# Optimization experiments

Measured on AMD Instinct MI355X. Metric: run time of the kernel, lower is better.

Reference implementation:

```python
import jax, jax.numpy as jnp
import numpy as np

M = 50000   # eval points
N = 1024    # gaussians
EPS = 1e-6


def setup_inputs() -> dict:
    key = jax.random.key(0)
    k1, k2, k3 = jax.random.split(key, 3)
    points = jax.random.uniform(k1, (M, 3), dtype=jnp.float32)          # normalized coords in [0,1)
    positions = jax.random.uniform(k2, (N, 3), dtype=jnp.float32)       # torch.rand init
    log_scales = jnp.full((N, 3), -3.0, dtype=jnp.float32)              # torch.full(..., -3.0)
    intensities = jax.random.uniform(k3, (N,), dtype=jnp.float32) * 0.5  # torch.rand * 0.5
    return {"points": points, "positions": positions,
            "log_scales": log_scales, "intensities": intensities}


def reference(points, positions, log_scales, intensities):
    # Faithful translation of FastGaussianModel._eval_gaussians
    scales = jnp.exp(log_scales)                      # [N,3]
    inv_var = 1.0 / (scales ** 2 + EPS)               # [N,3]
    diff = points[:, None, :] - positions[None, :, :] # [M,N,3]
    quad = jnp.einsum('mnd,nd->mn', diff * diff, inv_var)  # [M,N]
    gauss = jnp.exp(-0.5 * quad)                      # [M,N]
    values = gauss @ intensities                      # [M]
    return values
```

## Files before the change

kernel.cpp:

```cpp
#include <hip/hip_runtime.h>


typedef float v2f __attribute__((ext_vector_type(2)));

constexpr int NG_CHUNK = 128;
constexpr int BLOCK    = 256;

__global__ void fgm_prep(const float* __restrict__ positions,
                         const float* __restrict__ log_scales,
                         const float* __restrict__ intensities,
                         float* __restrict__ coef, int N, int Npad) {
    int n = blockIdx.x * blockDim.x + threadIdx.x;
    if (n >= Npad) return;
    float a0=0.f, a1=0.f, a2=0.f, b0=0.f, b1=0.f, b2=0.f, c=0.f, w=0.f;
    if (n < N) {
        const float K = -0.7213475204444817f;
        float q0 = positions[3*n+0], q1 = positions[3*n+1], q2 = positions[3*n+2];
        float iv0 = 1.0f / (__expf(2.0f*log_scales[3*n+0]) + 1e-6f);
        float iv1 = 1.0f / (__expf(2.0f*log_scales[3*n+1]) + 1e-6f);
        float iv2 = 1.0f / (__expf(2.0f*log_scales[3*n+2]) + 1e-6f);
        a0 = K * (-2.f*iv0*q0);  b0 = K * iv0;
        a1 = K * (-2.f*iv1*q1);  b1 = K * iv1;
        a2 = K * (-2.f*iv2*q2);  b2 = K * iv2;
        c  = K * (iv0*q0*q0 + iv1*q1*q1 + iv2*q2*q2);
        w  = intensities[n];
    }
    coef[0*Npad+n] = a0;  coef[1*Npad+n] = a1;  coef[2*Npad+n] = a2;
    coef[3*Npad+n] = b0;  coef[4*Npad+n] = b1;  coef[5*Npad+n] = b2;
    coef[6*Npad+n] = c;   coef[7*Npad+n] = w;
}

__global__ __launch_bounds__(BLOCK) void fgm_main(const float* __restrict__ points,
                                                  const float* __restrict__ coef,
                                                  float* __restrict__ out,
                                                  int M, int Npad) {
    int m = blockIdx.x * blockDim.x + threadIdx.x;
    float px = 0.f, py = 0.f, pz = 0.f;
    if (m < M) {
        px = points[3*m+0];
        py = points[3*m+1];
        pz = points[3*m+2];
    }
    v2f vpx  = {px, px},       vpy  = {py, py},       vpz  = {pz, pz};
    v2f vpx2 = {px*px, px*px}, vpy2 = {py*py, py*py}, vpz2 = {pz*pz, pz*pz};

    int half = blockIdx.y * (NG_CHUNK/2);
    const v2f* A0 = (const v2f*)(coef + 0*Npad) + half;
    const v2f* A1 = (const v2f*)(coef + 1*Npad) + half;
    const v2f* A2 = (const v2f*)(coef + 2*Npad) + half;
    const v2f* B0 = (const v2f*)(coef + 3*Npad) + half;
    const v2f* B1 = (const v2f*)(coef + 4*Npad) + half;
    const v2f* B2 = (const v2f*)(coef + 5*Npad) + half;
    const v2f* C  = (const v2f*)(coef + 6*Npad) + half;
    const v2f* W  = (const v2f*)(coef + 7*Npad) + half;

    v2f acc = {0.f, 0.f};
    #pragma unroll 4
    for (int i = 0; i < NG_CHUNK/2; ++i) {
        v2f t = __builtin_elementwise_fma(A0[i], vpx,  C[i]);
        t = __builtin_elementwise_fma(A1[i], vpy,  t);
        t = __builtin_elementwise_fma(A2[i], vpz,  t);
        t = __builtin_elementwise_fma(B0[i], vpx2, t);
        t = __builtin_elementwise_fma(B1[i], vpy2, t);
        t = __builtin_elementwise_fma(B2[i], vpz2, t);
        v2f g;
        g.x = __builtin_amdgcn_exp2f(t.x);
        g.y = __builtin_amdgcn_exp2f(t.y);
        acc = __builtin_elementwise_fma(g, W[i], acc);
    }
    if (m < M) atomicAdd(&out[m], acc.x + acc.y);
}

extern "C" void kernel_launch(void* const* d_in, const int* in_sizes, int n_in,
                              void* d_out, int out_size, void* d_ws, size_t ws_size,
                              hipStream_t stream) {
    const float* points      = (const float*)d_in[0];
    const float* positions   = (const float*)d_in[1];
    const float* log_scales  = (const float*)d_in[2];
    const float* intensities = (const float*)d_in[3];
    int M = in_sizes[0] / 3;
    int N = in_sizes[3];

    int chunks = (N + NG_CHUNK - 1) / NG_CHUNK;
    int Npad   = chunks * NG_CHUNK;

    float* coef = (float*)d_ws;

    hipMemsetAsync(d_out, 0, (size_t)out_size * sizeof(float), stream);

    fgm_prep<<<(Npad + 255) / 256, 256, 0, stream>>>(positions, log_scales,
                                                     intensities, coef, N, Npad);

    dim3 grid((M + BLOCK - 1) / BLOCK, chunks);
    fgm_main<<<grid, BLOCK, 0, stream>>>(points, coef, (float*)d_out, M, Npad);
}
```

Baseline: 77.07 us.

## Interleave coefficients per gaussian pair and drop N-splitting with atomics

The prep kernel now packs the eight coefficients of each gaussian pair contiguously as four float4s, so the main loop reads one contiguous 64-byte record per iteration instead of eight separate streams. The main kernel no longer splits the gaussians across a second grid dimension. Each 64-thread block loops over all pairs and writes its result directly, which removes the memset and the atomicAdds. The cost is a much smaller grid (about 782 single-wave blocks for 256 CUs) and longer per-thread loops, which reduces latency hiding and parallelism.

After: 105.2 us. +36.4%, slower.

```diff
diff --git a/kernel.cpp b/kernel.cpp
--- a/kernel.cpp
+++ b/kernel.cpp
@@ -3,38 +3,45 @@
 
 typedef float v2f __attribute__((ext_vector_type(2)));
 
-constexpr int NG_CHUNK = 128;
-constexpr int BLOCK    = 256;
+constexpr int BLOCK = 64;
 
 __global__ void fgm_prep(const float* __restrict__ positions,
                          const float* __restrict__ log_scales,
                          const float* __restrict__ intensities,
-                         float* __restrict__ coef, int N, int Npad) {
-    int n = blockIdx.x * blockDim.x + threadIdx.x;
-    if (n >= Npad) return;
-    float a0=0.f, a1=0.f, a2=0.f, b0=0.f, b1=0.f, b2=0.f, c=0.f, w=0.f;
-    if (n < N) {
-        const float K = -0.7213475204444817f;
-        float q0 = positions[3*n+0], q1 = positions[3*n+1], q2 = positions[3*n+2];
-        float iv0 = 1.0f / (__expf(2.0f*log_scales[3*n+0]) + 1e-6f);
-        float iv1 = 1.0f / (__expf(2.0f*log_scales[3*n+1]) + 1e-6f);
-        float iv2 = 1.0f / (__expf(2.0f*log_scales[3*n+2]) + 1e-6f);
-        a0 = K * (-2.f*iv0*q0);  b0 = K * iv0;
-        a1 = K * (-2.f*iv1*q1);  b1 = K * iv1;
-        a2 = K * (-2.f*iv2*q2);  b2 = K * iv2;
-        c  = K * (iv0*q0*q0 + iv1*q1*q1 + iv2*q2*q2);
-        w  = intensities[n];
+                         float* __restrict__ coef, int N, int Npairs) {
+    int i = blockIdx.x * blockDim.x + threadIdx.x;
+    if (i >= Npairs) return;
+    float v[2][8];
+    for (int h = 0; h < 2; ++h) {
+        int n = 2 * i + h;
+        float a0=0.f,a1=0.f,a2=0.f,b0=0.f,b1=0.f,b2=0.f,c=0.f,w=0.f;
+        if (n < N) {
+            const float K = -0.7213475204444817f;
+            float q0 = positions[3*n+0], q1 = positions[3*n+1], q2 = positions[3*n+2];
+            float iv0 = 1.0f / (__expf(2.0f*log_scales[3*n+0]) + 1e-6f);
+            float iv1 = 1.0f / (__expf(2.0f*log_scales[3*n+1]) + 1e-6f);
+            float iv2 = 1.0f / (__expf(2.0f*log_scales[3*n+2]) + 1e-6f);
+            a0 = K * (-2.f*iv0*q0);  b0 = K * iv0;
+            a1 = K * (-2.f*iv1*q1);  b1 = K * iv1;
+            a2 = K * (-2.f*iv2*q2);  b2 = K * iv2;
+            c  = K * (iv0*q0*q0 + iv1*q1*q1 + iv2*q2*q2);
+            w  = intensities[n];
+        }
+        v[h][0]=a0; v[h][1]=a1; v[h][2]=a2; v[h][3]=b0;
+        v[h][4]=b1; v[h][5]=b2; v[h][6]=c;  v[h][7]=w;
     }
-    coef[0*Npad+n] = a0;  coef[1*Npad+n] = a1;  coef[2*Npad+n] = a2;
-    coef[3*Npad+n] = b0;  coef[4*Npad+n] = b1;  coef[5*Npad+n] = b2;
-    coef[6*Npad+n] = c;   coef[7*Npad+n] = w;
+    float4* out = (float4*)(coef + (size_t)i * 16);
+    out[0] = make_float4(v[0][0], v[1][0], v[0][1], v[1][1]);
+    out[1] = make_float4(v[0][2], v[1][2], v[0][3], v[1][3]);
+    out[2] = make_float4(v[0][4], v[1][4], v[0][5], v[1][5]);
+    out[3] = make_float4(v[0][6], v[1][6], v[0][7], v[1][7]);
 }
 
 __global__ __launch_bounds__(BLOCK) void fgm_main(const float* __restrict__ points,
                                                   const float* __restrict__ coef,
                                                   float* __restrict__ out,
-                                                  int M, int Npad) {
-    int m = blockIdx.x * blockDim.x + threadIdx.x;
+                                                  int M, int Npairs) {
+    int m = blockIdx.x * BLOCK + threadIdx.x;
     float px = 0.f, py = 0.f, pz = 0.f;
     if (m < M) {
         px = points[3*m+0];
@@ -44,31 +51,24 @@
     v2f vpx  = {px, px},       vpy  = {py, py},       vpz  = {pz, pz};
     v2f vpx2 = {px*px, px*px}, vpy2 = {py*py, py*py}, vpz2 = {pz*pz, pz*pz};
 
-    int half = blockIdx.y * (NG_CHUNK/2);
-    const v2f* A0 = (const v2f*)(coef + 0*Npad) + half;
-    const v2f* A1 = (const v2f*)(coef + 1*Npad) + half;
-    const v2f* A2 = (const v2f*)(coef + 2*Npad) + half;
-    const v2f* B0 = (const v2f*)(coef + 3*Npad) + half;
-    const v2f* B1 = (const v2f*)(coef + 4*Npad) + half;
-    const v2f* B2 = (const v2f*)(coef + 5*Npad) + half;
-    const v2f* C  = (const v2f*)(coef + 6*Npad) + half;
-    const v2f* W  = (const v2f*)(coef + 7*Npad) + half;
-
+    const v2f* cp = (const v2f*)coef;
     v2f acc = {0.f, 0.f};
     #pragma unroll 4
-    for (int i = 0; i < NG_CHUNK/2; ++i) {
-        v2f t = __builtin_elementwise_fma(A0[i], vpx,  C[i]);
-        t = __builtin_elementwise_fma(A1[i], vpy,  t);
-        t = __builtin_elementwise_fma(A2[i], vpz,  t);
-        t = __builtin_elementwise_fma(B0[i], vpx2, t);
-        t = __builtin_elementwise_fma(B1[i], vpy2, t);
-        t = __builtin_elementwise_fma(B2[i], vpz2, t);
+    for (int i = 0; i < Npairs; ++i) {
+        v2f A0 = cp[8*i+0], A1 = cp[8*i+1], A2 = cp[8*i+2], B0 = cp[8*i+3];
+        v2f B1 = cp[8*i+4], B2 = cp[8*i+5], C  = cp[8*i+6], W  = cp[8*i+7];
+        v2f t = __builtin_elementwise_fma(A0, vpx,  C);
+        t = __builtin_elementwise_fma(A1, vpy,  t);
+        t = __builtin_elementwise_fma(A2, vpz,  t);
+        t = __builtin_elementwise_fma(B0, vpx2, t);
+        t = __builtin_elementwise_fma(B1, vpy2, t);
+        t = __builtin_elementwise_fma(B2, vpz2, t);
         v2f g;
         g.x = __builtin_amdgcn_exp2f(t.x);
         g.y = __builtin_amdgcn_exp2f(t.y);
-        acc = __builtin_elementwise_fma(g, W[i], acc);
+        acc = __builtin_elementwise_fma(g, W, acc);
     }
-    if (m < M) atomicAdd(&out[m], acc.x + acc.y);
+    if (m < M) out[m] = acc.x + acc.y;
 }
 
 extern "C" void kernel_launch(void* const* d_in, const int* in_sizes, int n_in,
@@ -81,16 +81,12 @@
     int M = in_sizes[0] / 3;
     int N = in_sizes[3];
 
-    int chunks = (N + NG_CHUNK - 1) / NG_CHUNK;
-    int Npad   = chunks * NG_CHUNK;
-
+    int Npairs = (N + 1) / 2;
     float* coef = (float*)d_ws;
 
-    hipMemsetAsync(d_out, 0, (size_t)out_size * sizeof(float), stream);
+    fgm_prep<<<(Npairs + 255) / 256, 256, 0, stream>>>(positions, log_scales,
+                                                       intensities, coef, N, Npairs);
 
-    fgm_prep<<<(Npad + 255) / 256, 256, 0, stream>>>(positions, log_scales,
-                                                     intensities, coef, N, Npad);
-
-    dim3 grid((M + BLOCK - 1) / BLOCK, chunks);
-    fgm_main<<<grid, BLOCK, 0, stream>>>(points, coef, (float*)d_out, M, Npad);
+    fgm_main<<<(M + BLOCK - 1) / BLOCK, BLOCK, 0, stream>>>(points, coef,
+                                                            (float*)d_out, M, Npairs);
 }
```
